# Performance work log

Hardware: AMD Instinct MI355X
Metric: run time of the kernel (lower is better)

## Reference

```python
import jax, jax.numpy as jnp
import numpy as np

B = 64
E = 512          # latent_size / h_dim
H = 8            # num_heads
D = E // H       # head_dim
MAX_AGENTS = 254 # max(agents_per_sample) for the deterministic counts below
NEG = -1e9


def setup_inputs() -> dict:
    key = jax.random.key(0)
    k_x, k_wi, k_bi, k_wo, k_bo = jax.random.split(key, 5)
    # deterministic variable agent counts in [128, 254]; sum == 11531, max == 254
    agents = jnp.array([128 + (3 * i) % 129 for i in range(B)], dtype=jnp.int32)
    total = 11531
    att_in = jax.random.normal(k_x, (total, E), dtype=jnp.float32)
    # nn.MultiheadAttention params: packed in-proj [3E, E] + bias, out-proj [E, E] + bias
    w_in = jax.random.normal(k_wi, (3 * E, E), dtype=jnp.float32) * 0.02
    b_in = jax.random.normal(k_bi, (3 * E,), dtype=jnp.float32) * 0.02
    w_out = jax.random.normal(k_wo, (E, E), dtype=jnp.float32) * 0.02
    b_out = jax.random.normal(k_bo, (E,), dtype=jnp.float32) * 0.02
    return {"att_in": att_in, "w_in": w_in, "b_in": b_in,
            "w_out": w_out, "b_out": b_out, "agents_per_sample": agents}


def reference(att_in, w_in, b_in, w_out, b_out, agents_per_sample):
    S = MAX_AGENTS
    # scatter packed rows into padded [B, S, E] via a clipped gather (jit-safe)
    offsets = jnp.cumsum(agents_per_sample) - agents_per_sample      # [B]
    pos = jnp.arange(S, dtype=jnp.int32)
    mask = pos[None, :] < agents_per_sample[:, None]                 # [B, S] valid
    idx = jnp.clip(offsets[:, None] + pos[None, :], 0, att_in.shape[0] - 1)
    padded = jnp.where(mask[..., None], att_in[idx], 0.0)            # [B, S, E]

    # fused QKV projection (torch packed in_proj), dropout disabled (eval)
    qkv = padded @ w_in.T + b_in                                     # [B, S, 3E]
    q, k, v = jnp.split(qkv, 3, axis=-1)
    q = q.reshape(B, S, H, D)
    k = k.reshape(B, S, H, D)
    v = v.reshape(B, S, H, D)

    scores = jnp.einsum('bqhd,bkhd->bhqk', q, k) * (D ** -0.5)      # [B, H, S, S]
    scores = jnp.where(mask[:, None, None, :], scores, NEG)          # key_padding_mask
    attn = jax.nn.softmax(scores, axis=-1)
    ctx = jnp.einsum('bhqk,bkhd->bqhd', attn, v).reshape(B, S, E)
    out = ctx @ w_out.T + b_out                                      # [B, S, E]
    # torch returns only valid rows per sample; zero the padded rows instead
    return out * mask[..., None]
```

## Files before the change

kernel.cpp:

```cpp
#include <hip/hip_runtime.h>
#include <hip/hip_bf16.h>

typedef __attribute__((ext_vector_type(8))) short bf16x8;
typedef __attribute__((ext_vector_type(4))) float f32x4;
typedef __attribute__((ext_vector_type(4))) int i32x4;
typedef __attribute__((ext_vector_type(4))) unsigned short u16x4;
typedef __attribute__((ext_vector_type(2))) unsigned ui2;
typedef __attribute__((ext_vector_type(4))) float fl4;

struct __attribute__((packed)) u16x4u { u16x4 v; };

__device__ __forceinline__ f32x4 mfma16(bf16x8 a, bf16x8 b, f32x4 c) {
    return __builtin_amdgcn_mfma_f32_16x16x32_bf16(a, b, c, 0, 0, 0);
}

__device__ __forceinline__ unsigned short f2b(float f) {
    unsigned u = __float_as_uint(f);
    unsigned r = (u + 0x7FFF + ((u >> 16) & 1)) >> 16;
    return (unsigned short)r;
}

__device__ __forceinline__ int bsearch_off(const int* s_off, int m) {
    int lo = 0, hi = 63;
    while (lo < hi) {
        int mid = (lo + hi + 1) >> 1;
        if (s_off[mid] <= m) lo = mid; else hi = mid - 1;
    }
    return lo;
}

__device__ __forceinline__ void gld_lds16(const __hip_bfloat16* g, __hip_bfloat16* l) {
    __builtin_amdgcn_global_load_lds(
        (const __attribute__((address_space(1))) void*)g,
        (__attribute__((address_space(3))) void*)l,
        16, 0, 0);
}

__global__ void k_prep(const unsigned short* __restrict__ src,
                       const void* __restrict__ b_in, const void* __restrict__ b_out,
                       const int* __restrict__ agents,
                       int* __restrict__ flag, int* __restrict__ offs,
                       float* __restrict__ bfi, float* __restrict__ bfo) {
    __shared__ int sh[256];
    __shared__ int sa[64];
    __shared__ int sflag;
    int tid = threadIdx.x;
    int h = 0;
    for (int i = tid; i < 16384; i += 256) {
        unsigned e = (src[i] >> 7) & 0xFF;
        if (e == 0xFF) h = 1;
    }
    sh[tid] = h;
    if (tid < 64) sa[tid] = agents[tid];
    __syncthreads();
    if (tid == 0) {
        int any = 0;
        for (int i = 0; i < 256; ++i) any |= sh[i];
        flag[0] = any;
        sflag = any;
    }
    if (tid < 64) {
        int ex = 0;
        for (int i = 0; i < 64; ++i) { int v = sa[i]; if (i < tid) ex += v; }
        offs[tid] = ex;
        if (tid == 63) offs[64] = ex + sa[63];
    }
    __syncthreads();
    int f = sflag;
    for (int i = tid; i < 1536; i += 256)
        bfi[i] = f ? ((const float*)b_in)[i]
                   : __bfloat162float(((const __hip_bfloat16*)b_in)[i]);
    for (int i = tid; i < 512; i += 256)
        bfo[i] = f ? ((const float*)b_out)[i]
                   : __bfloat162float(((const __hip_bfloat16*)b_out)[i]);
}

__global__ void k_zero_pad(char* __restrict__ out, const int* __restrict__ agents,
                           const int* __restrict__ flag) {
    int b = blockIdx.x;
    int n = agents[b];
    int esz = flag[0] ? 4 : 2;
    long long base = ((long long)b * 254 + n) * 512 * esz;
    long long bytes = (long long)(254 - n) * 512 * esz;
    for (long long i = ((long long)blockIdx.y * 256 + threadIdx.x) * 16;
         i < bytes; i += (long long)8 * 256 * 16)
        *(i32x4*)(out + base + i) = (i32x4){0, 0, 0, 0};
}

__global__ void k_cast_all(const void* __restrict__ sA, unsigned short* __restrict__ dA, int nA,
                           const void* __restrict__ sWi, unsigned short* __restrict__ dWi, int nWi,
                           const void* __restrict__ sWo, unsigned short* __restrict__ dWo, int nWo,
                           const int* __restrict__ flag) {
    int i = (blockIdx.x * 256 + threadIdx.x) * 4;
    const void* src; unsigned short* dst; int k;
    if (i < nA)            { src = sA;  dst = dA;  k = i; }
    else if (i < nA + nWi) { src = sWi; dst = dWi; k = i - nA; }
    else if (i < nA + nWi + nWo) { src = sWo; dst = dWo; k = i - nA - nWi; }
    else return;
    u16x4 o;
    if (flag[0]) {
        fl4 v = *(const fl4*)((const float*)src + k);
        o[0] = f2b(v[0]); o[1] = f2b(v[1]); o[2] = f2b(v[2]); o[3] = f2b(v[3]);
    } else {
        o = *(const u16x4*)((const unsigned short*)src + k);
    }
    *(u16x4*)(dst + k) = o;
}

template<int LDA, bool MROWS>
__device__ __forceinline__ void gemm_core(
    const __hip_bfloat16* __restrict__ A,
    const __hip_bfloat16* __restrict__ W,
    int m0, int n0, int total,
    __hip_bfloat16* As, __hip_bfloat16* Ws,
    f32x4 acc[4][4], int tid)
{
    int lane = tid & 63, quad = lane >> 4, c = lane & 15;
    int wave = tid >> 6;
    int wr = wave >> 1, wc = wave & 1;

    const __hip_bfloat16* gA[4];
    const __hip_bfloat16* gW[4];
    __hip_bfloat16* lA[4];
    __hip_bfloat16* lW[4];
#pragma unroll
    for (int j = 0; j < 4; ++j) {
        int L = j * 256 + tid;
        int row = L >> 3;
        int gseg = (L & 7) ^ (row & 7);
        int ar = m0 + row; if (ar > total - 1) ar = total - 1;
        gA[j] = A + (size_t)ar * LDA + gseg * 8;
        gW[j] = W + (size_t)(n0 + row) * 512 + gseg * 8;
        lA[j] = As + (size_t)(j * 256 + wave * 64) * 8;
        lW[j] = Ws + (size_t)(j * 256 + wave * 64) * 8;
    }

    for (int k0 = 0; k0 < 512; k0 += 64) {
        if (k0) __syncthreads();
#pragma unroll
        for (int j = 0; j < 4; ++j) gld_lds16(gA[j] + k0, lA[j]);
#pragma unroll
        for (int j = 0; j < 4; ++j) gld_lds16(gW[j] + k0, lW[j]);
        __syncthreads();
#pragma unroll
        for (int h = 0; h < 2; ++h) {
            bf16x8 af[4], wf[4];
#pragma unroll
            for (int t = 0; t < 4; ++t) {
                int rowa = wr * 64 + t * 16 + c;
                int rowb = wc * 64 + t * 16 + c;
                int ks = quad + 4 * h;
                af[t] = *(const bf16x8*)(As + (size_t)rowa * 64 + ((ks ^ (rowa & 7)) * 8));
                wf[t] = *(const bf16x8*)(Ws + (size_t)rowb * 64 + ((ks ^ (rowb & 7)) * 8));
            }
#pragma unroll
            for (int i = 0; i < 4; ++i)
#pragma unroll
                for (int j = 0; j < 4; ++j)
                    acc[i][j] = MROWS ? mfma16(af[i], wf[j], acc[i][j])
                                      : mfma16(wf[j], af[i], acc[i][j]);
        }
    }
}

__global__ __launch_bounds__(256) void k_qkv(
    const __hip_bfloat16* __restrict__ A,
    const __hip_bfloat16* __restrict__ W,
    const float* __restrict__ bias,
    const int* __restrict__ offs,
    __hip_bfloat16* __restrict__ qk,
    __hip_bfloat16* __restrict__ vT,
    int total, int MT)
{
    __shared__ __hip_bfloat16 As[128 * 64];
    __shared__ __hip_bfloat16 Ws[128 * 64];
    __shared__ int s_off[65];
    int l = blockIdx.x;
    int inner = l >> 3;
    int cb = inner % 12;
    int rb = (l & 7) + 8 * (inner / 12);
    if (rb >= MT) return;
    int n0 = cb * 128;
    int m0 = rb * 128;
    int tid = threadIdx.x;
    if (tid < 65) s_off[tid] = offs[tid];
    int lane = tid & 63, quad = lane >> 4, c = lane & 15;
    int wave = tid >> 6, wr = wave >> 1, wc = wave & 1;
    f32x4 z = {0.f, 0.f, 0.f, 0.f};
    f32x4 acc[4][4] = {{z,z,z,z},{z,z,z,z},{z,z,z,z},{z,z,z,z}};

    if (n0 < 1024) {
        gemm_core<512, false>(A, W, m0, n0, total, As, Ws, acc, tid);
        fl4 bv4[4];
#pragma unroll
        for (int j = 0; j < 4; ++j)
            bv4[j] = *(const fl4*)&bias[n0 + wc * 64 + j * 16 + quad * 4];
#pragma unroll
        for (int i = 0; i < 4; ++i) {
            int m = m0 + wr * 64 + i * 16 + c;
            if (m >= total) continue;
            size_t row = (size_t)m * 1024;
#pragma unroll
            for (int j = 0; j < 4; ++j) {
                int col0 = n0 + wc * 64 + j * 16 + quad * 4;
                u16x4 o;
#pragma unroll
                for (int r = 0; r < 4; ++r) o[r] = f2b(acc[i][j][r] + bv4[j][r]);
                *(u16x4*)&qk[row + col0] = o;
            }
        }
    } else {
        gemm_core<512, true>(A, W, m0, n0, total, As, Ws, acc, tid);
        float bv[4];
#pragma unroll
        for (int j = 0; j < 4; ++j) bv[j] = bias[n0 + wc * 64 + j * 16 + c];
#pragma unroll
        for (int i = 0; i < 4; ++i) {
            int m_base = m0 + wr * 64 + i * 16 + quad * 4;
            if (m_base >= total) continue;
            int lo = bsearch_off(s_off, m_base);
            bool vec = (m_base + 3 < total) && (s_off[lo + 1] > m_base + 3);
            if (vec) {
                int vs = m_base - s_off[lo];
#pragma unroll
                for (int j = 0; j < 4; ++j) {
                    int vc = n0 - 1024 + wc * 64 + j * 16 + c;
                    size_t idx = ((size_t)(lo * 8 + (vc >> 6)) * 64 + (vc & 63)) * 256 + vs;
                    u16x4 o;
#pragma unroll
                    for (int r = 0; r < 4; ++r) o[r] = f2b(acc[i][j][r] + bv[j]);
                    ((u16x4u*)&vT[idx])->v = o;
                }
            } else {
#pragma unroll
                for (int r = 0; r < 4; ++r) {
                    int m = m_base + r;
                    if (m >= total) continue;
                    int lo2 = bsearch_off(s_off, m);
                    int vs2 = m - s_off[lo2];
#pragma unroll
                    for (int j = 0; j < 4; ++j) {
                        int vc = n0 - 1024 + wc * 64 + j * 16 + c;
                        vT[((size_t)(lo2 * 8 + (vc >> 6)) * 64 + (vc & 63)) * 256 + vs2] =
                            __float2bfloat16(acc[i][j][r] + bv[j]);
                    }
                }
            }
        }
    }
}

__global__ __launch_bounds__(256, 2) void k_attn(
    __hip_bfloat16* __restrict__ qk,
    const __hip_bfloat16* __restrict__ vT,
    const int* __restrict__ agents,
    const int* __restrict__ offs)
{
    __shared__ __attribute__((aligned(16))) char Pl[4][16 * 80];
    int bh = blockIdx.x;
    int b = bh >> 3, h = bh & 7;
    int n = agents[b];
    int off = offs[b];
    int qtiles = (n + 15) >> 4;
    int stmax = (qtiles + 1) >> 1;
    int tid = threadIdx.x;
    int wave = tid >> 6, lane = tid & 63, quad = lane >> 4, c = lane & 15;
    const __hip_bfloat16* vbase = vT + (size_t)bh * 64 * 256;
    char* Plw = &Pl[wave][0];

    bf16x8 qB[4][2];
    int nt = 0;
#pragma unroll
    for (int t = 0; t < 4; ++t) {
        int qt = wave + 4 * t;
        if (qt < qtiles) {
            nt = t + 1;
            int qr = qt * 16 + c; if (qr > n - 1) qr = n - 1;
            const __hip_bfloat16* qp = qk + (size_t)(off + qr) * 1024 + h * 64 + quad * 8;
            qB[t][0] = *(const bf16x8*)qp;
            qB[t][1] = *(const bf16x8*)(qp + 32);
        }
    }

    f32x4 z = {0.f, 0.f, 0.f, 0.f};
    f32x4 O[4][4] = {{z,z,z,z},{z,z,z,z},{z,z,z,z},{z,z,z,z}};
    float sm[4] = {0.f, 0.f, 0.f, 0.f};
    const __hip_bfloat16* kg = qk + (size_t)off * 1024 + 512 + h * 64 + quad * 8;

    for (int st = 0; st < stmax; ++st) {
        int k0 = st * 32;
        bf16x8 kA[2][2];
#pragma unroll
        for (int ti = 0; ti < 2; ++ti) {
            int kr = k0 + ti * 16 + c; if (kr > n - 1) kr = n - 1;
            const __hip_bfloat16* kp = kg + (size_t)kr * 1024;
            kA[ti][0] = *(const bf16x8*)kp;
            kA[ti][1] = *(const bf16x8*)(kp + 32);
        }
        bf16x8 vA[4];
#pragma unroll
        for (int dt = 0; dt < 4; ++dt)
            vA[dt] = *(const bf16x8*)(vbase + (size_t)(dt * 16 + c) * 256 + k0 + quad * 8);

#pragma unroll
        for (int t = 0; t < 4; ++t) {
            if (t < nt) {
#pragma unroll
                for (int ti = 0; ti < 2; ++ti) {
                    f32x4 s = mfma16(kA[ti][0], qB[t][0], z);
                    s = mfma16(kA[ti][1], qB[t][1], s);
                    int kbase = k0 + ti * 16 + quad * 4;
                    float p0 = (kbase + 0 < n) ? __expf(s[0] * 0.125f) : 0.f;
                    float p1 = (kbase + 1 < n) ? __expf(s[1] * 0.125f) : 0.f;
                    float p2 = (kbase + 2 < n) ? __expf(s[2] * 0.125f) : 0.f;
                    float p3 = (kbase + 3 < n) ? __expf(s[3] * 0.125f) : 0.f;
                    sm[t] += (p0 + p1) + (p2 + p3);
                    ui2 dw;
                    dw[0] = (unsigned)f2b(p0) | ((unsigned)f2b(p1) << 16);
                    dw[1] = (unsigned)f2b(p2) | ((unsigned)f2b(p3) << 16);
                    *(ui2*)(Plw + c * 80 + ti * 32 + quad * 8) = dw;
                }
                bf16x8 pB = *(const bf16x8*)(Plw + c * 80 + quad * 16);
#pragma unroll
                for (int dt = 0; dt < 4; ++dt)
                    O[t][dt] = mfma16(vA[dt], pB, O[t][dt]);
            }
        }
    }

#pragma unroll
    for (int t = 0; t < 4; ++t) {
        if (t < nt) {
            float v = sm[t];
            v += __shfl_xor(v, 16);
            v += __shfl_xor(v, 32);
            float iv = 1.0f / v;
            int q = (wave + 4 * t) * 16 + c;
            if (q < n) {
                size_t row = (size_t)(off + q) * 1024 + h * 64;
#pragma unroll
                for (int dt = 0; dt < 4; ++dt) {
                    u16x4 o;
#pragma unroll
                    for (int r = 0; r < 4; ++r) o[r] = f2b(O[t][dt][r] * iv);
                    *(u16x4*)&qk[row + dt * 16 + quad * 4] = o;
                }
            }
        }
    }
}

__global__ __launch_bounds__(256) void k_out(
    const __hip_bfloat16* __restrict__ A,
    const __hip_bfloat16* __restrict__ W,
    const float* __restrict__ bias,
    const int* __restrict__ offs,
    void* __restrict__ out,
    const int* __restrict__ flag,
    int total, int MT)
{
    __shared__ __hip_bfloat16 As[128 * 64];
    __shared__ __hip_bfloat16 Ws[128 * 64];
    __shared__ int s_off[65];
    int l = blockIdx.x;
    int inner = l >> 3;
    int cb = inner & 3;
    int rb = (l & 7) + 8 * (inner >> 2);
    if (rb >= MT) return;
    int n0 = cb * 128;
    int m0 = rb * 128;
    int tid = threadIdx.x;
    if (tid < 65) s_off[tid] = offs[tid];
    f32x4 z = {0.f, 0.f, 0.f, 0.f};
    f32x4 acc[4][4] = {{z,z,z,z},{z,z,z,z},{z,z,z,z},{z,z,z,z}};
    gemm_core<1024, false>(A, W, m0, n0, total, As, Ws, acc, tid);

    int f32m = flag[0];
    int lane = tid & 63, quad = lane >> 4, c = lane & 15;
    int wave = tid >> 6, wr = wave >> 1, wc = wave & 1;
    fl4 bv4[4];
#pragma unroll
    for (int j = 0; j < 4; ++j)
        bv4[j] = *(const fl4*)&bias[n0 + wc * 64 + j * 16 + quad * 4];
#pragma unroll
    for (int i = 0; i < 4; ++i) {
        int m = m0 + wr * 64 + i * 16 + c;
        if (m >= total) continue;
        int lo = bsearch_off(s_off, m);
        int os_ = m - s_off[lo];
        size_t rowb = ((size_t)(lo * 254 + os_)) * 512;
#pragma unroll
        for (int j = 0; j < 4; ++j) {
            int col0 = n0 + wc * 64 + j * 16 + quad * 4;
            if (f32m) {
                fl4 o;
#pragma unroll
                for (int r = 0; r < 4; ++r) o[r] = acc[i][j][r] + bv4[j][r];
                *(fl4*)&((float*)out)[rowb + col0] = o;
            } else {
                u16x4 o;
#pragma unroll
                for (int r = 0; r < 4; ++r) o[r] = f2b(acc[i][j][r] + bv4[j][r]);
                *(u16x4*)&((__hip_bfloat16*)out)[rowb + col0] = o;
            }
        }
    }
}

extern "C" void kernel_launch(void* const* d_in, const int* in_sizes, int n_in,
                              void* d_out, int out_size, void* d_ws, size_t ws_size,
                              hipStream_t stream) {
    const void* att_in = d_in[0];
    const void* w_in   = d_in[1];
    const void* b_in   = d_in[2];
    const void* w_out  = d_in[3];
    const void* b_out  = d_in[4];
    const int* agents  = (const int*)d_in[5];
    int total = in_sizes[0] / 512;

    char* p = (char*)d_ws;
    int* flag  = (int*)p;                 p += 256;
    int* offs  = (int*)p;                 p += 512;
    float* bfi = (float*)p;               p += 1536 * 4;
    float* bfo = (float*)p;               p += 512 * 4;
    __hip_bfloat16* WinBf  = (__hip_bfloat16*)p;  p += (size_t)1536 * 512 * 2;
    __hip_bfloat16* WoutBf = (__hip_bfloat16*)p;  p += (size_t)512 * 512 * 2;
    __hip_bfloat16* Abf    = (__hip_bfloat16*)p;  p += (size_t)total * 512 * 2;
    __hip_bfloat16* qk     = (__hip_bfloat16*)p;  p += (size_t)total * 1024 * 2;
    __hip_bfloat16* vT     = (__hip_bfloat16*)p;  p += (size_t)64 * 8 * 64 * 256 * 2;

    int nA = total * 512, nWi = 1536 * 512, nWo = 512 * 512;
    int ntot = nA + nWi + nWo;

    k_prep<<<1, 256, 0, stream>>>((const unsigned short*)att_in, b_in, b_out,
                                  agents, flag, offs, bfi, bfo);
    k_zero_pad<<<dim3(64, 8), 256, 0, stream>>>((char*)d_out, agents, flag);
    k_cast_all<<<(ntot / 4 + 255) / 256, 256, 0, stream>>>(
        att_in, (unsigned short*)Abf, nA,
        w_in,   (unsigned short*)WinBf, nWi,
        w_out,  (unsigned short*)WoutBf, nWo, flag);

    int MT = (total + 127) / 128;
    int MTpad = ((MT + 7) / 8) * 8;
    k_qkv<<<12 * MTpad, 256, 0, stream>>>(Abf, WinBf, bfi, offs, qk, vT, total, MT);
    k_attn<<<512, 256, 0, stream>>>(qk, vT, agents, offs);
    k_out<<<4 * MTpad, 256, 0, stream>>>(qk, WoutBf, bfo, offs, d_out, flag, total, MT);
}
```

Measured before the change: 180.1 us.

## Replace LDS-staged GEMM tiles with direct global-to-register MFMA operand loads

```diff
diff --git a/kernel.cpp b/kernel.cpp
--- a/kernel.cpp
+++ b/kernel.cpp
@@ -27,13 +27,6 @@
         if (s_off[mid] <= m) lo = mid; else hi = mid - 1;
     }
     return lo;
-}
-
-__device__ __forceinline__ void gld_lds16(const __hip_bfloat16* g, __hip_bfloat16* l) {
-    __builtin_amdgcn_global_load_lds(
-        (const __attribute__((address_space(1))) void*)g,
-        (__attribute__((address_space(3))) void*)l,
-        16, 0, 0);
 }
 
 __global__ void k_prep(const unsigned short* __restrict__ src,
@@ -108,58 +101,36 @@
 }
 
 template<int LDA, bool MROWS>
-__device__ __forceinline__ void gemm_core(
+__device__ __forceinline__ void gemm_direct(
     const __hip_bfloat16* __restrict__ A,
     const __hip_bfloat16* __restrict__ W,
     int m0, int n0, int total,
-    __hip_bfloat16* As, __hip_bfloat16* Ws,
     f32x4 acc[4][4], int tid)
 {
     int lane = tid & 63, quad = lane >> 4, c = lane & 15;
     int wave = tid >> 6;
     int wr = wave >> 1, wc = wave & 1;
-
-    const __hip_bfloat16* gA[4];
-    const __hip_bfloat16* gW[4];
-    __hip_bfloat16* lA[4];
-    __hip_bfloat16* lW[4];
-#pragma unroll
-    for (int j = 0; j < 4; ++j) {
-        int L = j * 256 + tid;
-        int row = L >> 3;
-        int gseg = (L & 7) ^ (row & 7);
-        int ar = m0 + row; if (ar > total - 1) ar = total - 1;
-        gA[j] = A + (size_t)ar * LDA + gseg * 8;
-        gW[j] = W + (size_t)(n0 + row) * 512 + gseg * 8;
-        lA[j] = As + (size_t)(j * 256 + wave * 64) * 8;
-        lW[j] = Ws + (size_t)(j * 256 + wave * 64) * 8;
-    }
-
-    for (int k0 = 0; k0 < 512; k0 += 64) {
-        if (k0) __syncthreads();
-#pragma unroll
-        for (int j = 0; j < 4; ++j) gld_lds16(gA[j] + k0, lA[j]);
-#pragma unroll
-        for (int j = 0; j < 4; ++j) gld_lds16(gW[j] + k0, lW[j]);
-        __syncthreads();
-#pragma unroll
-        for (int h = 0; h < 2; ++h) {
-            bf16x8 af[4], wf[4];
-#pragma unroll
-            for (int t = 0; t < 4; ++t) {
-                int rowa = wr * 64 + t * 16 + c;
-                int rowb = wc * 64 + t * 16 + c;
-                int ks = quad + 4 * h;
-                af[t] = *(const bf16x8*)(As + (size_t)rowa * 64 + ((ks ^ (rowa & 7)) * 8));
-                wf[t] = *(const bf16x8*)(Ws + (size_t)rowb * 64 + ((ks ^ (rowb & 7)) * 8));
-            }
-#pragma unroll
-            for (int i = 0; i < 4; ++i)
-#pragma unroll
-                for (int j = 0; j < 4; ++j)
-                    acc[i][j] = MROWS ? mfma16(af[i], wf[j], acc[i][j])
-                                      : mfma16(wf[j], af[i], acc[i][j]);
-        }
+    const __hip_bfloat16* Ap[4];
+    const __hip_bfloat16* Wp[4];
+#pragma unroll
+    for (int t = 0; t < 4; ++t) {
+        int ar = m0 + wr * 64 + t * 16 + c; if (ar > total - 1) ar = total - 1;
+        Ap[t] = A + (size_t)ar * LDA + quad * 8;
+        Wp[t] = W + (size_t)(n0 + wc * 64 + t * 16 + c) * 512 + quad * 8;
+    }
+#pragma unroll
+    for (int k0 = 0; k0 < 512; k0 += 32) {
+        bf16x8 af[4], wf[4];
+#pragma unroll
+        for (int t = 0; t < 4; ++t) af[t] = *(const bf16x8*)(Ap[t] + k0);
+#pragma unroll
+        for (int t = 0; t < 4; ++t) wf[t] = *(const bf16x8*)(Wp[t] + k0);
+#pragma unroll
+        for (int i = 0; i < 4; ++i)
+#pragma unroll
+            for (int j = 0; j < 4; ++j)
+                acc[i][j] = MROWS ? mfma16(af[i], wf[j], acc[i][j])
+                                  : mfma16(wf[j], af[i], acc[i][j]);
     }
 }
 
@@ -172,8 +143,6 @@
     __hip_bfloat16* __restrict__ vT,
     int total, int MT)
 {
-    __shared__ __hip_bfloat16 As[128 * 64];
-    __shared__ __hip_bfloat16 Ws[128 * 64];
     __shared__ int s_off[65];
     int l = blockIdx.x;
     int inner = l >> 3;
@@ -190,7 +159,7 @@
     f32x4 acc[4][4] = {{z,z,z,z},{z,z,z,z},{z,z,z,z},{z,z,z,z}};
 
     if (n0 < 1024) {
-        gemm_core<512, false>(A, W, m0, n0, total, As, Ws, acc, tid);
+        gemm_direct<512, false>(A, W, m0, n0, total, acc, tid);
         fl4 bv4[4];
 #pragma unroll
         for (int j = 0; j < 4; ++j)
@@ -210,7 +179,8 @@
             }
         }
     } else {
-        gemm_core<512, true>(A, W, m0, n0, total, As, Ws, acc, tid);
+        gemm_direct<512, true>(A, W, m0, n0, total, acc, tid);
+        __syncthreads();
         float bv[4];
 #pragma unroll
         for (int j = 0; j < 4; ++j) bv[j] = bias[n0 + wc * 64 + j * 16 + c];
@@ -359,8 +329,6 @@
     const int* __restrict__ flag,
     int total, int MT)
 {
-    __shared__ __hip_bfloat16 As[128 * 64];
-    __shared__ __hip_bfloat16 Ws[128 * 64];
     __shared__ int s_off[65];
     int l = blockIdx.x;
     int inner = l >> 3;
@@ -373,7 +341,8 @@
     if (tid < 65) s_off[tid] = offs[tid];
     f32x4 z = {0.f, 0.f, 0.f, 0.f};
     f32x4 acc[4][4] = {{z,z,z,z},{z,z,z,z},{z,z,z,z},{z,z,z,z}};
-    gemm_core<1024, false>(A, W, m0, n0, total, As, Ws, acc, tid);
+    gemm_direct<1024, false>(A, W, m0, n0, total, acc, tid);
+    __syncthreads();
 
     int f32m = flag[0];
     int lane = tid & 63, quad = lane >> 4, c = lane & 15;
```

Result: slower. 243.2 us (+35.0%).
